# Performance work log

Measured on AMD Instinct MI355X. Metric: run time of the kernel, lower is better.

The kernel has to match this reference:

```python
import jax, jax.numpy as jnp
import numpy as np
import jax.scipy.linalg as jsl


def _rbf(X1, X2, log_lengthscale):
    # squared-exponential kernel: exp(-0.5 * ||x1 - x2||^2 / ls^2)
    ls2 = jnp.exp(2.0 * log_lengthscale)
    d2 = (jnp.sum(X1 * X1, axis=1)[:, None]
          + jnp.sum(X2 * X2, axis=1)[None, :]
          - 2.0 * (X1 @ X2.T))
    return jnp.exp(-0.5 * jnp.maximum(d2, 0.0) / ls2)


def setup_inputs() -> dict:
    key = jax.random.key(0)
    k1, k2, k3, k4, k5 = jax.random.split(key, 5)
    N, D, l, rank, N_ = 1024, 8, 4, 2, 1024
    return {
        "X": jax.random.normal(k1, (N, D), dtype=jnp.float32),
        "test_X": jax.random.normal(k2, (N_, D), dtype=jnp.float32),
        "Y": jax.random.normal(k3, (N, l), dtype=jnp.float32),
        "log_noise": jnp.zeros((l,), dtype=jnp.float32),
        "covar_factor": jax.random.normal(k4, (l, rank), dtype=jnp.float32),
        "log_var": jax.random.normal(k5, (l,), dtype=jnp.float32),
        "log_lengthscale": jnp.zeros((), dtype=jnp.float32),
    }


def reference(X, test_X, Y, log_noise, covar_factor, log_var, log_lengthscale):
    N, l = Y.shape
    N_ = test_X.shape[0]
    # IndexKernel: B B^T + diag(exp(log_var))   -> (l, l)
    task_K = covar_factor @ covar_factor.T + jnp.diag(jnp.exp(log_var))
    # per-task noise kron identity -> (N*l, N*l)
    noise = jnp.kron(jnp.diag(jnp.exp(log_noise)), jnp.eye(N, dtype=X.dtype))
    # full Kronecker covariance and its Cholesky factor
    K = jnp.kron(task_K, _rbf(X, X, log_lengthscale)) + noise
    L = jnp.linalg.cholesky(K)                       # (N*l, N*l), lower
    Kx = jnp.kron(task_K, _rbf(X, test_X, log_lengthscale))     # (N*l, N_*l)
    Kxx = jnp.kron(task_K, _rbf(test_X, test_X, log_lengthscale))  # (N_*l, N_*l)
    A = jsl.solve_triangular(L, Kx, lower=True)      # L A = Kx
    Y_vec = Y.T.reshape(-1, 1)                        # vec of Y^T, (N*l, 1)
    V = jsl.solve_triangular(L, Y_vec, lower=True)
    fmean = A.T @ V                                   # (N_*l, 1)
    fvar = Kxx - A.T @ A                              # (N_*l, N_*l)
    return fmean, fvar, noise, fmean.reshape(l, N_).T
```

## Files before the change

### kernel.cpp

```cpp
#include <hip/hip_runtime.h>
#include <math.h>

#define NN 1024
#define NM (NN*NN)
#define NB 64
#define NBLK 16
#define NW 1152
#define BIG 4096

#define OFF_FVAR  ((size_t)4096)
#define OFF_NOISE ((size_t)(4096 + 16777216))
#define OFF_M4    ((size_t)(4096 + 2*16777216))

struct GPParams {
  float tk[16];
  float E[16];
  float G[16];
  float lam[4];
};

__global__ void k_prep(const float* __restrict__ logn, const float* __restrict__ cf,
                       const float* __restrict__ logv, GPParams* __restrict__ P)
{
  if (threadIdx.x != 0 || blockIdx.x != 0) return;
  double tk[4][4], Dn[4], T[4][4], U[4][4];
  for (int a=0;a<4;a++) for (int b=0;b<4;b++){
    double s = 0.0;
    for (int r=0;r<2;r++) s += (double)cf[a*2+r]*(double)cf[b*2+r];
    if (a==b) s += exp((double)logv[a]);
    tk[a][b] = s;
  }
  for (int a=0;a<4;a++) Dn[a] = exp((double)logn[a]);
  for (int a=0;a<4;a++) for (int b=0;b<4;b++)
    T[a][b] = tk[a][b]/sqrt(Dn[a]*Dn[b]);
  for (int a=0;a<4;a++) for (int b=0;b<4;b++) U[a][b] = (a==b)?1.0:0.0;
  for (int sweep=0; sweep<40; sweep++){
    for (int p=0;p<3;p++) for (int q=p+1;q<4;q++){
      double apq = T[p][q];
      if (fabs(apq) < 1e-300) continue;
      double tau = (T[q][q]-T[p][p])/(2.0*apq);
      double t = (tau >= 0.0) ? 1.0/(tau + sqrt(1.0+tau*tau))
                              : 1.0/(tau - sqrt(1.0+tau*tau));
      double c = 1.0/sqrt(1.0+t*t), s = t*c;
      for (int k=0;k<4;k++){ double akp=T[k][p], akq=T[k][q];
        T[k][p]=c*akp - s*akq; T[k][q]=s*akp + c*akq; }
      for (int k=0;k<4;k++){ double apk=T[p][k], aqk=T[q][k];
        T[p][k]=c*apk - s*aqk; T[q][k]=s*apk + c*aqk; }
      for (int k=0;k<4;k++){ double ukp=U[k][p], ukq=U[k][q];
        U[k][p]=c*ukp - s*ukq; U[k][q]=s*ukp + c*ukq; }
    }
  }
  double E[4][4], G[4][4];
  for (int a=0;a<4;a++) for (int i=0;i<4;i++) E[a][i] = U[a][i]/sqrt(Dn[a]);
  for (int a=0;a<4;a++) for (int i=0;i<4;i++){
    double s=0; for (int b=0;b<4;b++) s += tk[a][b]*E[b][i];
    G[a][i]=s;
  }
  for (int a=0;a<4;a++) for (int b=0;b<4;b++){
    P->tk[a*4+b] = (float)tk[a][b];
    P->E [a*4+b] = (float)E[a][b];
    P->G [a*4+b] = (float)G[a][b];
  }
  for (int i=0;i<4;i++){
    double l = T[i][i];
    P->lam[i] = (float)(l > 0.0 ? l : 0.0);
  }
}

__global__ void k_rbf(const float* __restrict__ X1, const float* __restrict__ X2,
                      const float* __restrict__ logls, float* __restrict__ out)
{
  __shared__ float x1s[16][8];
  __shared__ float x2s[16][8];
  int tx = threadIdx.x, ty = threadIdx.y;
  int tid = ty*16 + tx;
  if (tid < 128){
    int r = tid>>3, d = tid&7;
    x1s[r][d] = X1[((size_t)blockIdx.y*16 + r)*8 + d];
  } else {
    int t2 = tid-128, r = t2>>3, d = t2&7;
    x2s[r][d] = X2[((size_t)blockIdx.x*16 + r)*8 + d];
  }
  __syncthreads();
  float ls2 = expf(2.0f*logls[0]);
  float d2 = 0.f;
  #pragma unroll
  for (int d=0; d<8; d++){ float df = x1s[ty][d]-x2s[tx][d]; d2 += df*df; }
  int i = blockIdx.y*16+ty, j = blockIdx.x*16+tx;
  out[(size_t)i*NN + j] = expf(-0.5f*d2/ls2);
}

__global__ void k_rbfM(const float* __restrict__ X1, const float* __restrict__ logls,
                       const GPParams* __restrict__ P, float* __restrict__ M)
{
  __shared__ float x1s[16][8];
  __shared__ float x2s[16][8];
  int tx = threadIdx.x, ty = threadIdx.y;
  int tid = ty*16 + tx;
  if (tid < 128){
    int r = tid>>3, d = tid&7;
    x1s[r][d] = X1[((size_t)blockIdx.y*16 + r)*8 + d];
  } else {
    int t2 = tid-128, r = t2>>3, d = t2&7;
    x2s[r][d] = X1[((size_t)blockIdx.x*16 + r)*8 + d];
  }
  __syncthreads();
  float ls2 = expf(2.0f*logls[0]);
  float d2 = 0.f;
  #pragma unroll
  for (int d=0; d<8; d++){ float df = x1s[ty][d]-x2s[tx][d]; d2 += df*df; }
  int i = blockIdx.y*16+ty, j = blockIdx.x*16+tx;
  float v = expf(-0.5f*d2/ls2);
  float diag = (i==j) ? 1.f : 0.f;
  size_t idx = (size_t)i*NN + j;
  #pragma unroll
  for (int z=0;z<4;z++)
    M[(size_t)z*NM + idx] = P->lam[z]*v + diag;
}

__global__ void k_uvec(const float* __restrict__ Y, const GPParams* __restrict__ P,
                       float* __restrict__ u)
{
  int n = blockIdx.x*256 + threadIdx.x;
  float y0 = Y[n*4+0], y1 = Y[n*4+1], y2 = Y[n*4+2], y3 = Y[n*4+3];
  #pragma unroll
  for (int i=0;i<4;i++)
    u[i*NN + n] = P->E[0*4+i]*y0 + P->E[1*4+i]*y1 + P->E[2*4+i]*y2 + P->E[3*4+i]*y3;
}

__device__ __forceinline__ void gemm64(const float* __restrict__ A, const float* __restrict__ B,
                                       float acc[4][4], int r0, int c0, bool sub)
{
  for (int p=0;p<64;p++){
    float ar[4], bc[4];
    #pragma unroll
    for (int ii=0;ii<4;ii++) ar[ii]=A[(r0+ii)*65+p];
    #pragma unroll
    for (int jj=0;jj<4;jj++) bc[jj]=B[p*65+c0+jj];
    if (sub){
      #pragma unroll
      for (int ii=0;ii<4;ii++)
        #pragma unroll
        for (int jj=0;jj<4;jj++) acc[ii][jj] -= ar[ii]*bc[jj];
    } else {
      #pragma unroll
      for (int ii=0;ii<4;ii++)
        #pragma unroll
        for (int jj=0;jj<4;jj++) acc[ii][jj] += ar[ii]*bc[jj];
    }
  }
}

__global__ __launch_bounds__(256) void k_potf2(float* __restrict__ M, float* __restrict__ Linv, int k)
{
  int z = blockIdx.x, tid = threadIdx.x;
  __shared__ float a[64*65];
  __shared__ float lo[64*65];
  __shared__ float ai[32*33];
  __shared__ float bb[32*33];
  __shared__ float t1[32*33];
  float* Mz = M + (size_t)z*NM;
  int base = k*NB;
  for (int idx=tid; idx<4096; idx+=256){
    int r=idx>>6, c=idx&63;
    a[r*65+c] = Mz[(size_t)(base+r)*NN + base + c];
  }
  int r = tid & 63, q = tid >> 6;
  for (int j=0;j<64;j++){
    __syncthreads();
    float d = a[j*65+j];
    float invd = 1.f/d;
    float rs = rsqrtf(d);
    if (q==0){
      if (r == j) lo[j*65+j] = sqrtf(d);
      else if (r > j) lo[r*65+j] = a[r*65+j]*rs;
      else lo[r*65+j] = 0.f;
    }
    if (r > j){
      float lrj = a[r*65+j]*invd;
      for (int c=j+1+q; c<=r; c+=4)
        a[r*65+c] -= lrj * a[c*65+j];
    }
  }
  __syncthreads();
  if (tid < 32){
    int c = tid;
    for (int rr=0;rr<c;rr++) ai[rr*33+c]=0.f;
    for (int rr=c;rr<32;rr++){
      float s = (rr==c)?1.f:0.f;
      for (int j=c;j<rr;j++) s -= lo[rr*65+j]*ai[j*33+c];
      ai[rr*33+c] = s / lo[rr*65+rr];
    }
  } else if (tid < 64){
    int c = tid-32;
    for (int rr=0;rr<c;rr++) bb[rr*33+c]=0.f;
    for (int rr=c;rr<32;rr++){
      float s=(rr==c)?1.f:0.f;
      for (int j=c;j<rr;j++) s -= lo[(32+rr)*65+(32+j)]*bb[j*33+c];
      bb[rr*33+c] = s / lo[(32+rr)*65+(32+rr)];
    }
  }
  __syncthreads();
  for (int idx=tid; idx<1024; idx+=256){
    int rr=idx>>5, c=idx&31;
    float s=0.f;
    for (int j=0;j<32;j++) s += lo[(32+rr)*65+j]*ai[j*33+c];
    t1[rr*33+c]=s;
  }
  __syncthreads();
  float* Lg = Linv + ((size_t)z*NBLK + k)*(NB*NB);
  float* Td = Mz + (size_t)base*NN + base;
  for (int idx=tid; idx<1024; idx+=256){
    int rr=idx>>5, c=idx&31;
    float s=0.f;
    for (int j=0;j<32;j++) s += bb[rr*33+j]*t1[j*33+c];
    float q21 = -s, q11 = ai[rr*33+c], q22 = bb[rr*33+c];
    Lg[(32+rr)*64 + c]      = q21;
    Lg[rr*64 + (32+c)]      = 0.f;
    Lg[rr*64 + c]           = q11;
    Lg[(32+rr)*64 + (32+c)] = q22;
    Td[(size_t)(32+rr)*NN + c]      = q21;
    Td[(size_t)rr*NN + (32+c)]      = 0.f;
    Td[(size_t)rr*NN + c]           = q11;
    Td[(size_t)(32+rr)*NN + (32+c)] = q22;
  }
}

__global__ __launch_bounds__(256) void k_csf(float* __restrict__ M, float* __restrict__ Linv,
                                             float* __restrict__ Lbuf, int k)
{
  int z = blockIdx.z;
  int tt = blockIdx.x, i2 = 0;
  while (tt >= i2+1){ tt -= (i2+1); i2++; }
  int bi = k+1+i2, bj = k+1+tt;
  bool fblk = (i2==0);
  bool diag = (bi==bj);
  __shared__ float pa[64*65];
  __shared__ float pb[64*65];
  __shared__ float li[64*65];
  float* Mz = M + (size_t)z*NM;
  const float* Lg = Linv + ((size_t)z*NBLK + k)*(NB*NB);
  int tid = threadIdx.x;
  for (int idx=tid; idx<4096; idx+=256){
    int r=idx>>6, c=idx&63;
    li[r*65+c] = Lg[idx];
    pa[r*65+c] = Mz[(size_t)(bi*64+r)*NN + k*64 + c];
    if (fblk)       pb[r*65+c] = Mz[(size_t)(bi*64+r)*NN + bi*64 + c];
    else if (!diag) pb[r*65+c] = Mz[(size_t)(bj*64+r)*NN + k*64 + c];
  }
  __syncthreads();
  int r0 = tid & 63, qq = tid >> 6;
  float sp[16], sq[16];
  for (int s=0;s<16;s++){
    int c = qq + s*4;
    float acc=0.f;
    for (int p=0;p<=c;p++) acc += pa[r0*65+p]*li[c*65+p];
    sp[s]=acc;
  }
  if (!diag){
    for (int s=0;s<16;s++){
      int c = qq + s*4;
      float acc=0.f;
      for (int p=0;p<=c;p++) acc += pb[r0*65+p]*li[c*65+p];
      sq[s]=acc;
    }
  }
  __syncthreads();
  for (int s=0;s<16;s++){
    int c = qq + s*4;
    pa[r0*65+c]=sp[s];
    if (!diag) pb[r0*65+c]=sq[s];
  }
  __syncthreads();
  float acc[4][4] = {};
  int ty = tid>>4, tx = tid&15;
  int rr0 = ty*4, cc0 = tx*4;
  const float* pbb = diag ? pa : pb;
  for (int p=0;p<64;p++){
    float ar[4], bc[4];
    #pragma unroll
    for (int ii=0;ii<4;ii++) ar[ii]=pa[(rr0+ii)*65+p];
    #pragma unroll
    for (int jj=0;jj<4;jj++) bc[jj]=pbb[(cc0+jj)*65+p];
    #pragma unroll
    for (int ii=0;ii<4;ii++)
      #pragma unroll
      for (int jj=0;jj<4;jj++) acc[ii][jj] += ar[ii]*bc[jj];
  }

  if (!fblk){
    for (int ii=0;ii<4;ii++){
      float4* ptr = (float4*)&Mz[(size_t)(bi*64+rr0+ii)*NN + bj*64+cc0];
      float4 v = *ptr;
      v.x-=acc[ii][0]; v.y-=acc[ii][1]; v.z-=acc[ii][2]; v.w-=acc[ii][3];
      *ptr = v;
    }
    if (bj == k+1){
      float* Lb = Lbuf + (size_t)z*NM;
      for (int idx=tid; idx<4096; idx+=256){
        int r=idx>>6, c=idx&63;
        Lb[(size_t)(bi*64+r)*NN + k*64 + c] = pa[r*65+c];
      }
    }
    return;
  }

  #pragma unroll
  for (int ii=0;ii<4;ii++)
    #pragma unroll
    for (int jj=0;jj<4;jj++) pb[(rr0+ii)*65+cc0+jj] -= acc[ii][jj];
  {
    float* Lb = Lbuf + (size_t)z*NM;
    for (int idx=tid; idx<4096; idx+=256){
      int r=idx>>6, c=idx&63;
      Lb[(size_t)(bi*64+r)*NN + k*64 + c] = pa[r*65+c];
    }
  }
  int r = tid & 63, q = tid >> 6;
  for (int j=0;j<64;j++){
    __syncthreads();
    float d = pb[j*65+j];
    float invd = 1.f/d;
    float rs = rsqrtf(d);
    if (q==0){
      if (r == j) li[j*65+j] = sqrtf(d);
      else if (r > j) li[r*65+j] = pb[r*65+j]*rs;
      else li[r*65+j] = 0.f;
    }
    if (r > j){
      float lrj = pb[r*65+j]*invd;
      for (int c=j+1+q; c<=r; c+=4)
        pb[r*65+c] -= lrj * pb[c*65+j];
    }
  }
  __syncthreads();
  float* ai = pa;
  float* bb = pa + 1056;
  float* t1 = pa + 2112;
  if (tid < 32){
    int c = tid;
    for (int rr=0;rr<c;rr++) ai[rr*33+c]=0.f;
    for (int rr=c;rr<32;rr++){
      float s = (rr==c)?1.f:0.f;
      for (int j=c;j<rr;j++) s -= li[rr*65+j]*ai[j*33+c];
      ai[rr*33+c] = s / li[rr*65+rr];
    }
  } else if (tid < 64){
    int c = tid-32;
    for (int rr=0;rr<c;rr++) bb[rr*33+c]=0.f;
    for (int rr=c;rr<32;rr++){
      float s=(rr==c)?1.f:0.f;
      for (int j=c;j<rr;j++) s -= li[(32+rr)*65+(32+j)]*bb[j*33+c];
      bb[rr*33+c] = s / li[(32+rr)*65+(32+rr)];
    }
  }
  __syncthreads();
  for (int idx=tid; idx<1024; idx+=256){
    int rr=idx>>5, c=idx&31;
    float s=0.f;
    for (int j=0;j<32;j++) s += li[(32+rr)*65+j]*ai[j*33+c];
    t1[rr*33+c]=s;
  }
  __syncthreads();
  float* Lg2 = Linv + ((size_t)z*NBLK + (k+1))*(NB*NB);
  float* Td  = Mz + (size_t)(bi*64)*NN + bi*64;
  for (int idx=tid; idx<1024; idx+=256){
    int rr=idx>>5, c=idx&31;
    float s=0.f;
    for (int j=0;j<32;j++) s += bb[rr*33+j]*t1[j*33+c];
    float q21 = -s, q11 = ai[rr*33+c], q22 = bb[rr*33+c];
    Lg2[(32+rr)*64 + c]      = q21;
    Lg2[rr*64 + (32+c)]      = 0.f;
    Lg2[rr*64 + c]           = q11;
    Lg2[(32+rr)*64 + (32+c)] = q22;
    Td[(size_t)(32+rr)*NN + c]      = q21;
    Td[(size_t)rr*NN + (32+c)]      = 0.f;
    Td[(size_t)rr*NN + c]           = q11;
    Td[(size_t)(32+rr)*NN + (32+c)] = q22;
  }
}

__global__ __launch_bounds__(256) void k_dbl1(const float* __restrict__ Lbuf,
                                              const float* __restrict__ Linv,
                                              float* __restrict__ Tinv)
{
  int pair = blockIdx.x, z = blockIdx.y, tid = threadIdx.x;
  int b0 = 2*pair, b1 = 2*pair+1;
  __shared__ float l21[64*65];
  __shared__ float ai[64*65];
  __shared__ float tt[64*65];
  const float* Lb = Lbuf + (size_t)z*NM;
  const float* La = Linv + ((size_t)z*NBLK + b0)*(NB*NB);
  const float* Lc = Linv + ((size_t)z*NBLK + b1)*(NB*NB);
  for (int idx=tid; idx<4096; idx+=256){
    int r=idx>>6, c=idx&63;
    l21[r*65+c] = Lb[(size_t)(b1*64+r)*NN + b0*64 + c];
    ai[r*65+c]  = La[idx];
  }
  __syncthreads();
  int ty=tid>>4, tx=tid&15, r0=ty*4, c0=tx*4;
  float acc[4][4]={};
  gemm64(l21, ai, acc, r0, c0, false);
  __syncthreads();
  #pragma unroll
  for (int ii=0;ii<4;ii++)
    #pragma unroll
    for (int jj=0;jj<4;jj++) tt[(r0+ii)*65 + c0+jj] = acc[ii][jj];
  for (int idx=tid; idx<4096; idx+=256){
    int r=idx>>6, c=idx&63;
    ai[r*65+c] = Lc[idx];
  }
  __syncthreads();
  float fin[4][4]={};
  gemm64(ai, tt, fin, r0, c0, false);
  float* Tz = Tinv + (size_t)z*NM;
  #pragma unroll
  for (int ii=0;ii<4;ii++){
    float4 v = make_float4(-fin[ii][0],-fin[ii][1],-fin[ii][2],-fin[ii][3]);
    *(float4*)&Tz[(size_t)(b1*64+r0+ii)*NN + b0*64+c0] = v;
  }
}

__global__ __launch_bounds__(256) void k_dblT(const float* __restrict__ Lbuf,
                                              const float* __restrict__ Tinv,
                                              float* __restrict__ tb, int g64)
{
  int z = blockIdx.y, tid = threadIdx.x;
  int tpp = g64*g64;
  int pair = blockIdx.x / tpp;
  int tt2 = blockIdx.x % tpp;
  int ti = tt2 / g64, tj = tt2 % g64;
  int b0 = 2*pair*g64, b1 = b0 + g64;
  const float* Lb = Lbuf + (size_t)z*NM;
  const float* Tz = Tinv + (size_t)z*NM;
  __shared__ float lt[64*65];
  __shared__ float rt[64*65];
  int ty=tid>>4, tx=tid&15, r0=ty*4, c0=tx*4;
  float acc[4][4]={};
  for (int kb=tj; kb<g64; kb++){
    for (int idx=tid; idx<4096; idx+=256){
      int r=idx>>6, c=idx&63;
      lt[r*65+c] = Lb[(size_t)((b1+ti)*64+r)*NN + (b0+kb)*64 + c];
      rt[r*65+c] = Tz[(size_t)((b0+kb)*64+r)*NN + (b0+tj)*64 + c];
    }
    __syncthreads();
    gemm64(lt, rt, acc, r0, c0, false);
    __syncthreads();
  }
  int g = g64*64;
  float* tz = tb + (size_t)z*262144 + (size_t)pair*g*g;
  #pragma unroll
  for (int ii=0;ii<4;ii++){
    float4 v = make_float4(acc[ii][0],acc[ii][1],acc[ii][2],acc[ii][3]);
    *(float4*)&tz[(size_t)(ti*64+r0+ii)*g + tj*64+c0] = v;
  }
}

__global__ __launch_bounds__(256) void k_dblC(const float* __restrict__ tb,
                                              float* __restrict__ Tinv, int g64)
{
  int z = blockIdx.y, tid = threadIdx.x;
  int tpp = g64*g64;
  int pair = blockIdx.x / tpp;
  int tt2 = blockIdx.x % tpp;
  int ti = tt2 / g64, tj = tt2 % g64;
  int b0 = 2*pair*g64, b1 = b0 + g64;
  float* Tz = Tinv + (size_t)z*NM;
  int g = g64*64;
  const float* tz = tb + (size_t)z*262144 + (size_t)pair*g*g;
  __shared__ float lt[64*65];
  __shared__ float rt[64*65];
  int ty=tid>>4, tx=tid&15, r0=ty*4, c0=tx*4;
  float acc[4][4]={};
  for (int kb=0; kb<=ti; kb++){
    for (int idx=tid; idx<4096; idx+=256){
      int r=idx>>6, c=idx&63;
      lt[r*65+c] = Tz[(size_t)((b1+ti)*64+r)*NN + (b1+kb)*64 + c];
      rt[r*65+c] = tz[(size_t)(kb*64+r)*g + tj*64 + c];
    }
    __syncthreads();
    gemm64(lt, rt, acc, r0, c0, false);
    __syncthreads();
  }
  #pragma unroll
  for (int ii=0;ii<4;ii++){
    float4 v = make_float4(-acc[ii][0],-acc[ii][1],-acc[ii][2],-acc[ii][3]);
    *(float4*)&Tz[(size_t)((b1+ti)*64+r0+ii)*NN + b0*64+tj*64+c0] = v;
  }
}

__global__ __launch_bounds__(256) void k_wgemm(const float* __restrict__ Tinv,
                                               const float* __restrict__ R,
                                               const float* __restrict__ u,
                                               float* __restrict__ W)
{
  int ct = blockIdx.x;
  int bi = blockIdx.y;
  int z  = blockIdx.z;
  const float* Tz = Tinv + (size_t)z*NM;
  float* Wz = W + (size_t)z*NN*NW;
  __shared__ float At[64*68];
  __shared__ float Bs[64*132];
  int tid = threadIdx.x;
  int ty = tid>>4, tx = tid&15;
  float areg[16], breg[32];
  float acc[4][8] = {};
  #pragma unroll
  for (int i=0;i<16;i++){
    int idx=i*256+tid, r=idx>>6, c=idx&63;
    areg[i] = Tz[(size_t)(bi*64+r)*NN + c];
  }
  #pragma unroll
  for (int i=0;i<32;i++){
    int idx=i*256+tid, r=idx>>7, c=idx&127;
    breg[i] = (ct<8) ? R[(size_t)r*NN + ct*128 + c]
                     : ((c<4) ? u[c*NN + r] : 0.f);
  }
  for (int kb=0; kb<=bi; kb++){
    __syncthreads();
    #pragma unroll
    for (int i=0;i<16;i++){
      int idx=i*256+tid, r=idx>>6, c=idx&63;
      At[c*68 + r] = areg[i];
    }
    #pragma unroll
    for (int i=0;i<32;i++){
      int idx=i*256+tid, r=idx>>7, c=idx&127;
      Bs[r*132 + c] = breg[i];
    }
    if (kb < bi){
      int kn = kb+1;
      #pragma unroll
      for (int i=0;i<16;i++){
        int idx=i*256+tid, r=idx>>6, c=idx&63;
        areg[i] = Tz[(size_t)(bi*64+r)*NN + kn*64 + c];
      }
      #pragma unroll
      for (int i=0;i<32;i++){
        int idx=i*256+tid, r=idx>>7, c=idx&127;
        int gr = kn*64 + r;
        breg[i] = (ct<8) ? R[(size_t)gr*NN + ct*128 + c]
                         : ((c<4) ? u[c*NN + gr] : 0.f);
      }
    }
    __syncthreads();
    for (int p=0;p<64;p++){
      float4 a4 = *(const float4*)&At[p*68 + ty*4];
      float4 b0 = *(const float4*)&Bs[p*132 + tx*8];
      float4 b1 = *(const float4*)&Bs[p*132 + tx*8 + 4];
      float ar[4]={a4.x,a4.y,a4.z,a4.w};
      float bc[8]={b0.x,b0.y,b0.z,b0.w,b1.x,b1.y,b1.z,b1.w};
      #pragma unroll
      for (int ii=0;ii<4;ii++)
        #pragma unroll
        for (int jj=0;jj<8;jj++) acc[ii][jj] += ar[ii]*bc[jj];
    }
  }
  #pragma unroll
  for (int ii=0;ii<4;ii++){
    size_t row = (size_t)(bi*64 + ty*4 + ii)*NW + ct*128 + tx*8;
    *(float4*)&Wz[row]   = make_float4(acc[ii][0],acc[ii][1],acc[ii][2],acc[ii][3]);
    *(float4*)&Wz[row+4] = make_float4(acc[ii][4],acc[ii][5],acc[ii][6],acc[ii][7]);
  }
}

__global__ __launch_bounds__(256) void k_WtW(const float* __restrict__ W,
                                             float* __restrict__ Qa, float* __restrict__ Qb)
{
  int z = blockIdx.z;
  int ks = blockIdx.x / 36;
  int tt = blockIdx.x % 36, mi = 0;
  while (tt >= mi+1){ tt -= (mi+1); mi++; }
  int mj = tt;
  const float* Wz = W + (size_t)z*NN*NW;
  float* Qz = (ks ? Qb : Qa) + (size_t)z*NM;
  int mi0 = mi*128, mj0 = mj*128;
  __shared__ float as[16*132];
  __shared__ float bs[16*132];
  int tid = threadIdx.x;
  int ty = tid>>4, tx = tid&15;
  float areg[8], breg[8];
  float acc[8][8] = {};
  int nbase = ks*512;
  #pragma unroll
  for (int i=0;i<8;i++){
    int idx=i*256+tid, r=idx>>7, c=idx&127;
    areg[i] = Wz[(size_t)(nbase+r)*NW + mi0 + c];
    breg[i] = Wz[(size_t)(nbase+r)*NW + mj0 + c];
  }
  for (int s=0;s<32;s++){
    __syncthreads();
    #pragma unroll
    for (int i=0;i<8;i++){
      int idx=i*256+tid, r=idx>>7, c=idx&127;
      as[r*132+c]=areg[i];
      bs[r*132+c]=breg[i];
    }
    if (s<31){
      int n0 = nbase + (s+1)*16;
      #pragma unroll
      for (int i=0;i<8;i++){
        int idx=i*256+tid, r=idx>>7, c=idx&127;
        areg[i] = Wz[(size_t)(n0+r)*NW + mi0 + c];
        breg[i] = Wz[(size_t)(n0+r)*NW + mj0 + c];
      }
    }
    __syncthreads();
    #pragma unroll
    for (int p=0;p<16;p++){
      float4 a0 = *(const float4*)&as[p*132 + ty*8];
      float4 a1 = *(const float4*)&as[p*132 + ty*8 + 4];
      float4 b0 = *(const float4*)&bs[p*132 + tx*8];
      float4 b1 = *(const float4*)&bs[p*132 + tx*8 + 4];
      float arf[8]={a0.x,a0.y,a0.z,a0.w,a1.x,a1.y,a1.z,a1.w};
      float bcf[8]={b0.x,b0.y,b0.z,b0.w,b1.x,b1.y,b1.z,b1.w};
      #pragma unroll
      for (int ii=0;ii<8;ii++)
        #pragma unroll
        for (int jj=0;jj<8;jj++) acc[ii][jj]+=arf[ii]*bcf[jj];
    }
  }
  for (int ii=0;ii<8;ii++){
    size_t row = (size_t)(mi0 + ty*8 + ii)*NN + mj0 + tx*8;
    *(float4*)&Qz[row]   = make_float4(acc[ii][0],acc[ii][1],acc[ii][2],acc[ii][3]);
    *(float4*)&Qz[row+4] = make_float4(acc[ii][4],acc[ii][5],acc[ii][6],acc[ii][7]);
  }
  if (mi != mj){
    for (int jj=0;jj<8;jj++){
      size_t row = (size_t)(mj0 + tx*8 + jj)*NN + mi0 + ty*8;
      *(float4*)&Qz[row]   = make_float4(acc[0][jj],acc[1][jj],acc[2][jj],acc[3][jj]);
      *(float4*)&Qz[row+4] = make_float4(acc[4][jj],acc[5][jj],acc[6][jj],acc[7][jj]);
    }
  }
}

__global__ void k_colmul(const float* __restrict__ W, float* __restrict__ wpart)
{
  int mc = blockIdx.x, z = blockIdx.y, ns = blockIdx.z, tid = threadIdx.x;
  __shared__ float ufs[256];
  const float* Wz = W + (size_t)z*NN*NW;
  ufs[tid] = Wz[(size_t)(ns*256+tid)*NW + 1024 + z];
  __syncthreads();
  int m = mc*256 + tid;
  float acc = 0.f;
  for (int n=0;n<256;n++)
    acc += Wz[(size_t)(ns*256+n)*NW + m]*ufs[n];
  wpart[(size_t)(z*4+ns)*1024 + m] = acc;
}

__global__ void k_fmeanout(const float* __restrict__ wpart, const GPParams* __restrict__ P,
                           float* __restrict__ out)
{
  int m = blockIdx.x*256 + threadIdx.x;
  float w[4];
  #pragma unroll
  for (int i=0;i<4;i++){
    float s=0.f;
    #pragma unroll
    for (int ns=0;ns<4;ns++) s += wpart[(size_t)(i*4+ns)*1024 + m];
    w[i]=s;
  }
  #pragma unroll
  for (int a=0;a<4;a++){
    float fm = 0.f;
    #pragma unroll
    for (int i=0;i<4;i++) fm += P->G[a*4+i]*w[i];
    out[a*NN + m] = fm;
    out[OFF_M4 + (size_t)m*4 + a] = fm;
  }
}

__global__ void k_fvar(const float* __restrict__ S, const float* __restrict__ Qa,
                       const float* __restrict__ Qb, const GPParams* __restrict__ P,
                       float* __restrict__ out)
{
  size_t idx = (size_t)blockIdx.x*256 + threadIdx.x;
  int m = (int)(idx>>10), mp = (int)(idx & 1023);
  float s = S[idx];
  float q[4];
  #pragma unroll
  for (int i=0;i<4;i++) q[i] = Qa[(size_t)i*NM + idx] + Qb[(size_t)i*NM + idx];
  float* fv = out + OFF_FVAR;
  #pragma unroll
  for (int a=0;a<4;a++)
    #pragma unroll
    for (int b=0;b<4;b++){
      float val = P->tk[a*4+b]*s;
      #pragma unroll
      for (int i=0;i<4;i++) val -= P->G[a*4+i]*P->G[b*4+i]*q[i];
      fv[(size_t)(a*NN+m)*BIG + (size_t)b*NN + mp] = val;
    }
}

__global__ void k_noise(const float* __restrict__ logn, float* __restrict__ out)
{
  size_t idx = (size_t)blockIdx.x*256 + threadIdx.x;
  int row = (int)(idx>>12), col = (int)(idx & 4095);
  out[OFF_NOISE + idx] = (row==col) ? expf(logn[row>>10]) : 0.f;
}

extern "C" void kernel_launch(void* const* d_in, const int* in_sizes, int n_in,
                              void* d_out, int out_size, void* d_ws, size_t ws_size,
                              hipStream_t stream)
{
  const float* X    = (const float*)d_in[0];
  const float* tX   = (const float*)d_in[1];
  const float* Y    = (const float*)d_in[2];
  const float* logn = (const float*)d_in[3];
  const float* cf   = (const float*)d_in[4];
  const float* logv = (const float*)d_in[5];
  const float* logls= (const float*)d_in[6];
  float* out = (float*)d_out;

  size_t need_floats = 64 + 4096 + 16384
                     + 2*(size_t)NM + 4*(size_t)NM + 262144 + 4*(size_t)NM
                     + 4*(size_t)NN*NW;
  float* base;
  if (ws_size >= (need_floats + 1024)*sizeof(float)) base = (float*)d_ws;
  else base = out + OFF_NOISE;

  GPParams* P  = (GPParams*)base;
  float* u     = base + 64;
  float* wpart = u + 4096;
  float* R     = wpart + 16384;
  float* S     = R + NM;
  float* M     = S + NM;
  float* Linv  = M + 4*(size_t)NM;
  float* Lbuf  = Linv + 262144;
  float* W     = Lbuf + 4*(size_t)NM;
  float* Tinv  = M;
  float* Qa    = M;
  float* Qb    = Lbuf;
  float* tb    = W;

  dim3 b16(16,16);

  k_prep<<<1, 1, 0, stream>>>(logn, cf, logv, P);
  k_rbf <<<dim3(64,64), b16, 0, stream>>>(X,  tX, logls, R);
  k_rbf <<<dim3(64,64), b16, 0, stream>>>(tX, tX, logls, S);
  k_rbfM<<<dim3(64,64), b16, 0, stream>>>(X, logls, P, M);
  k_uvec<<<dim3(4), 256, 0, stream>>>(Y, P, u);

  k_potf2<<<dim3(4), 256, 0, stream>>>(M, Linv, 0);
  for (int k=0;k<NBLK-1;k++){
    int nb = NBLK-1-k;
    k_csf<<<dim3(nb*(nb+1)/2, 1, 4), 256, 0, stream>>>(M, Linv, Lbuf, k);
  }

  k_dbl1<<<dim3(8,4), 256, 0, stream>>>(Lbuf, Linv, Tinv);
  for (int g64=2; g64<=8; g64*=2){
    int np = 8/g64;
    k_dblT<<<dim3(np*g64*g64, 4), 256, 0, stream>>>(Lbuf, Tinv, tb, g64);
    k_dblC<<<dim3(np*g64*g64, 4), 256, 0, stream>>>(tb, Tinv, g64);
  }

  k_wgemm<<<dim3(9,16,4), 256, 0, stream>>>(Tinv, R, u, W);

  k_WtW<<<dim3(72,1,4), 256, 0, stream>>>(W, Qa, Qb);
  k_colmul<<<dim3(4,4,4), 256, 0, stream>>>(W, wpart);
  k_fmeanout<<<dim3(4), 256, 0, stream>>>(wpart, P, out);
  k_fvar<<<dim3(NM/256), 256, 0, stream>>>(S, Qa, Qb, P, out);
  k_noise<<<dim3(16777216/256), 256, 0, stream>>>(logn, out);
}
```

Measured before the change: 2.296 ms.

## Use precomputed Linv^T Linv for trailing updates and split-K WtW with atomics

The right-looking blocked Cholesky now precomputes G = Linv_k^T Linv_k for each diagonal block. Trailing-update blocks then compute A_i G A_j^T with dense 64x64 GEMMs instead of triangular solves on both panels. Panel solves are done only where L is actually stored: the first sub-diagonal block and the bj==k+1 column. Separately, the WtW reduction is split four ways along K and accumulated with atomicAdd into a zeroed Q, which doubles parallelism but adds a zeroing pass, atomic traffic, nondeterministic summation order, and extra flops in the Cholesky.

```diff
diff --git a/kernel.cpp b/kernel.cpp
--- a/kernel.cpp
+++ b/kernel.cpp
@@ -150,8 +150,24 @@
     }
   }
 }
-
-__global__ __launch_bounds__(256) void k_potf2(float* __restrict__ M, float* __restrict__ Linv, int k)
+__device__ __forceinline__ void gemm64T(const float* __restrict__ A, const float* __restrict__ B,
+                                        float acc[4][4], int r0, int c0)
+{
+  for (int p=0;p<64;p++){
+    float ar[4], bc[4];
+    #pragma unroll
+    for (int ii=0;ii<4;ii++) ar[ii]=A[(r0+ii)*65+p];
+    #pragma unroll
+    for (int jj=0;jj<4;jj++) bc[jj]=B[(c0+jj)*65+p];
+    #pragma unroll
+    for (int ii=0;ii<4;ii++)
+      #pragma unroll
+      for (int jj=0;jj<4;jj++) acc[ii][jj] += ar[ii]*bc[jj];
+  }
+}
+
+__global__ __launch_bounds__(256) void k_potf2(float* __restrict__ M, float* __restrict__ Linv,
+                                               float* __restrict__ Gbuf, int k)
 {
   int z = blockIdx.x, tid = threadIdx.x;
   __shared__ float a[64*65];
@@ -223,160 +239,204 @@
     Td[(size_t)rr*NN + (32+c)]      = 0.f;
     Td[(size_t)rr*NN + c]           = q11;
     Td[(size_t)(32+rr)*NN + (32+c)] = q22;
+    a[(32+rr)*65 + c]      = q21;
+    a[rr*65 + (32+c)]      = 0.f;
+    a[rr*65 + c]           = q11;
+    a[(32+rr)*65 + (32+c)] = q22;
+  }
+  __syncthreads();
+  {
+    int r0=(tid>>4)*4, c0=(tid&15)*4;
+    float g[4][4]={};
+    for (int p=0;p<64;p++){
+      float ar[4], bc[4];
+      #pragma unroll
+      for (int ii=0;ii<4;ii++) ar[ii]=a[p*65+r0+ii];
+      #pragma unroll
+      for (int jj=0;jj<4;jj++) bc[jj]=a[p*65+c0+jj];
+      #pragma unroll
+      for (int ii=0;ii<4;ii++)
+        #pragma unroll
+        for (int jj=0;jj<4;jj++) g[ii][jj]+=ar[ii]*bc[jj];
+    }
+    float* Gg = Gbuf + ((size_t)z*NBLK + k)*4096;
+    #pragma unroll
+    for (int ii=0;ii<4;ii++)
+      *(float4*)&Gg[(r0+ii)*64 + c0] = make_float4(g[ii][0],g[ii][1],g[ii][2],g[ii][3]);
   }
 }
 
 __global__ __launch_bounds__(256) void k_csf(float* __restrict__ M, float* __restrict__ Linv,
-                                             float* __restrict__ Lbuf, int k)
+                                             float* __restrict__ Gbuf, float* __restrict__ Lbuf, int k)
 {
   int z = blockIdx.z;
   int tt = blockIdx.x, i2 = 0;
   while (tt >= i2+1){ tt -= (i2+1); i2++; }
   int bi = k+1+i2, bj = k+1+tt;
   bool fblk = (i2==0);
-  bool diag = (bi==bj);
   __shared__ float pa[64*65];
   __shared__ float pb[64*65];
   __shared__ float li[64*65];
   float* Mz = M + (size_t)z*NM;
-  const float* Lg = Linv + ((size_t)z*NBLK + k)*(NB*NB);
+  float* Lb = Lbuf + (size_t)z*NM;
   int tid = threadIdx.x;
+  int ty = tid>>4, tx = tid&15;
+  int r0 = ty*4, c0 = tx*4;
+
+  if (fblk){
+    const float* Lg = Linv + ((size_t)z*NBLK + k)*(NB*NB);
+    for (int idx=tid; idx<4096; idx+=256){
+      int r=idx>>6, c=idx&63;
+      li[r*65+c] = Lg[idx];
+      pa[r*65+c] = Mz[(size_t)(bi*64+r)*NN + k*64 + c];
+      pb[r*65+c] = Mz[(size_t)(bi*64+r)*NN + bi*64 + c];
+    }
+    __syncthreads();
+    float sc[4][4]={};
+    gemm64T(pa, li, sc, r0, c0);
+    #pragma unroll
+    for (int ii=0;ii<4;ii++)
+      *(float4*)&Lb[(size_t)(bi*64+r0+ii)*NN + k*64+c0] =
+        make_float4(sc[ii][0],sc[ii][1],sc[ii][2],sc[ii][3]);
+    __syncthreads();
+    #pragma unroll
+    for (int ii=0;ii<4;ii++)
+      #pragma unroll
+      for (int jj=0;jj<4;jj++) pa[(r0+ii)*65+c0+jj] = sc[ii][jj];
+    __syncthreads();
+    float upd[4][4]={};
+    gemm64T(pa, pa, upd, r0, c0);
+    #pragma unroll
+    for (int ii=0;ii<4;ii++)
+      #pragma unroll
+      for (int jj=0;jj<4;jj++) pb[(r0+ii)*65+c0+jj] -= upd[ii][jj];
+    int r = tid & 63, q = tid >> 6;
+    for (int j=0;j<64;j++){
+      __syncthreads();
+      float d = pb[j*65+j];
+      float invd = 1.f/d;
+      float rs = rsqrtf(d);
+      if (q==0){
+        if (r == j) li[j*65+j] = sqrtf(d);
+        else if (r > j) li[r*65+j] = pb[r*65+j]*rs;
+        else li[r*65+j] = 0.f;
+      }
+      if (r > j){
+        float lrj = pb[r*65+j]*invd;
+        for (int c=j+1+q; c<=r; c+=4)
+          pb[r*65+c] -= lrj * pb[c*65+j];
+      }
+    }
+    __syncthreads();
+    float* ai = pa;
+    float* bbv = pa + 1056;
+    float* t1 = pa + 2112;
+    if (tid < 32){
+      int c = tid;
+      for (int rr=0;rr<c;rr++) ai[rr*33+c]=0.f;
+      for (int rr=c;rr<32;rr++){
+        float s = (rr==c)?1.f:0.f;
+        for (int j=c;j<rr;j++) s -= li[rr*65+j]*ai[j*33+c];
+        ai[rr*33+c] = s / li[rr*65+rr];
+      }
+    } else if (tid < 64){
+      int c = tid-32;
+      for (int rr=0;rr<c;rr++) bbv[rr*33+c]=0.f;
+      for (int rr=c;rr<32;rr++){
+        float s=(rr==c)?1.f:0.f;
+        for (int j=c;j<rr;j++) s -= li[(32+rr)*65+(32+j)]*bbv[j*33+c];
+        bbv[rr*33+c] = s / li[(32+rr)*65+(32+rr)];
+      }
+    }
+    __syncthreads();
+    for (int idx=tid; idx<1024; idx+=256){
+      int rr=idx>>5, c=idx&31;
+      float s=0.f;
+      for (int j=0;j<32;j++) s += li[(32+rr)*65+j]*ai[j*33+c];
+      t1[rr*33+c]=s;
+    }
+    __syncthreads();
+    float* Lg2 = Linv + ((size_t)z*NBLK + (k+1))*(NB*NB);
+    float* Td  = Mz + (size_t)(bi*64)*NN + bi*64;
+    for (int idx=tid; idx<1024; idx+=256){
+      int rr=idx>>5, c=idx&31;
+      float s=0.f;
+      for (int j=0;j<32;j++) s += bbv[rr*33+j]*t1[j*33+c];
+      float q21 = -s, q11 = ai[rr*33+c], q22 = bbv[rr*33+c];
+      Lg2[(32+rr)*64 + c]      = q21;
+      Lg2[rr*64 + (32+c)]      = 0.f;
+      Lg2[rr*64 + c]           = q11;
+      Lg2[(32+rr)*64 + (32+c)] = q22;
+      Td[(size_t)(32+rr)*NN + c]      = q21;
+      Td[(size_t)rr*NN + (32+c)]      = 0.f;
+      Td[(size_t)rr*NN + c]           = q11;
+      Td[(size_t)(32+rr)*NN + (32+c)] = q22;
+      pb[(32+rr)*65 + c]      = q21;
+      pb[rr*65 + (32+c)]      = 0.f;
+      pb[rr*65 + c]           = q11;
+      pb[(32+rr)*65 + (32+c)] = q22;
+    }
+    __syncthreads();
+    {
+      float g[4][4]={};
+      for (int p=0;p<64;p++){
+        float ar[4], bc[4];
+        #pragma unroll
+        for (int ii=0;ii<4;ii++) ar[ii]=pb[p*65+r0+ii];
+        #pragma unroll
+        for (int jj=0;jj<4;jj++) bc[jj]=pb[p*65+c0+jj];
+        #pragma unroll
+        for (int ii=0;ii<4;ii++)
+          #pragma unroll
+          for (int jj=0;jj<4;jj++) g[ii][jj]+=ar[ii]*bc[jj];
+      }
+      float* Gg = Gbuf + ((size_t)z*NBLK + (k+1))*4096;
+      #pragma unroll
+      for (int ii=0;ii<4;ii++)
+        *(float4*)&Gg[(r0+ii)*64 + c0] = make_float4(g[ii][0],g[ii][1],g[ii][2],g[ii][3]);
+    }
+    return;
+  }
+
+  const float* Gg = Gbuf + ((size_t)z*NBLK + k)*4096;
   for (int idx=tid; idx<4096; idx+=256){
     int r=idx>>6, c=idx&63;
-    li[r*65+c] = Lg[idx];
+    li[r*65+c] = Gg[idx];
     pa[r*65+c] = Mz[(size_t)(bi*64+r)*NN + k*64 + c];
-    if (fblk)       pb[r*65+c] = Mz[(size_t)(bi*64+r)*NN + bi*64 + c];
-    else if (!diag) pb[r*65+c] = Mz[(size_t)(bj*64+r)*NN + k*64 + c];
-  }
-  __syncthreads();
-  int r0 = tid & 63, qq = tid >> 6;
-  float sp[16], sq[16];
-  for (int s=0;s<16;s++){
-    int c = qq + s*4;
-    float acc=0.f;
-    for (int p=0;p<=c;p++) acc += pa[r0*65+p]*li[c*65+p];
-    sp[s]=acc;
-  }
-  if (!diag){
-    for (int s=0;s<16;s++){
-      int c = qq + s*4;
-      float acc=0.f;
-      for (int p=0;p<=c;p++) acc += pb[r0*65+p]*li[c*65+p];
-      sq[s]=acc;
-    }
-  }
-  __syncthreads();
-  for (int s=0;s<16;s++){
-    int c = qq + s*4;
-    pa[r0*65+c]=sp[s];
-    if (!diag) pb[r0*65+c]=sq[s];
-  }
-  __syncthreads();
-  float acc[4][4] = {};
-  int ty = tid>>4, tx = tid&15;
-  int rr0 = ty*4, cc0 = tx*4;
-  const float* pbb = diag ? pa : pb;
-  for (int p=0;p<64;p++){
-    float ar[4], bc[4];
-    #pragma unroll
-    for (int ii=0;ii<4;ii++) ar[ii]=pa[(rr0+ii)*65+p];
-    #pragma unroll
-    for (int jj=0;jj<4;jj++) bc[jj]=pbb[(cc0+jj)*65+p];
-    #pragma unroll
-    for (int ii=0;ii<4;ii++)
-      #pragma unroll
-      for (int jj=0;jj<4;jj++) acc[ii][jj] += ar[ii]*bc[jj];
-  }
-
-  if (!fblk){
-    for (int ii=0;ii<4;ii++){
-      float4* ptr = (float4*)&Mz[(size_t)(bi*64+rr0+ii)*NN + bj*64+cc0];
-      float4 v = *ptr;
-      v.x-=acc[ii][0]; v.y-=acc[ii][1]; v.z-=acc[ii][2]; v.w-=acc[ii][3];
-      *ptr = v;
-    }
-    if (bj == k+1){
-      float* Lb = Lbuf + (size_t)z*NM;
-      for (int idx=tid; idx<4096; idx+=256){
-        int r=idx>>6, c=idx&63;
-        Lb[(size_t)(bi*64+r)*NN + k*64 + c] = pa[r*65+c];
-      }
-    }
-    return;
-  }
-
+    pb[r*65+c] = Mz[(size_t)(bj*64+r)*NN + k*64 + c];
+  }
+  __syncthreads();
+  float t[4][4]={};
+  gemm64(pa, li, t, r0, c0, false);
+  __syncthreads();
   #pragma unroll
   for (int ii=0;ii<4;ii++)
     #pragma unroll
-    for (int jj=0;jj<4;jj++) pb[(rr0+ii)*65+cc0+jj] -= acc[ii][jj];
-  {
-    float* Lb = Lbuf + (size_t)z*NM;
+    for (int jj=0;jj<4;jj++) li[(r0+ii)*65+c0+jj] = t[ii][jj];
+  __syncthreads();
+  float upd[4][4]={};
+  gemm64T(li, pb, upd, r0, c0);
+  #pragma unroll
+  for (int ii=0;ii<4;ii++){
+    float4* ptr = (float4*)&Mz[(size_t)(bi*64+r0+ii)*NN + bj*64+c0];
+    float4 v = *ptr;
+    v.x-=upd[ii][0]; v.y-=upd[ii][1]; v.z-=upd[ii][2]; v.w-=upd[ii][3];
+    *ptr = v;
+  }
+  if (bj == k+1){
+    __syncthreads();
+    const float* Lg = Linv + ((size_t)z*NBLK + k)*(NB*NB);
     for (int idx=tid; idx<4096; idx+=256){
       int r=idx>>6, c=idx&63;
-      Lb[(size_t)(bi*64+r)*NN + k*64 + c] = pa[r*65+c];
-    }
-  }
-  int r = tid & 63, q = tid >> 6;
-  for (int j=0;j<64;j++){
-    __syncthreads();
-    float d = pb[j*65+j];
-    float invd = 1.f/d;
-    float rs = rsqrtf(d);
-    if (q==0){
-      if (r == j) li[j*65+j] = sqrtf(d);
-      else if (r > j) li[r*65+j] = pb[r*65+j]*rs;
-      else li[r*65+j] = 0.f;
-    }
-    if (r > j){
-      float lrj = pb[r*65+j]*invd;
-      for (int c=j+1+q; c<=r; c+=4)
-        pb[r*65+c] -= lrj * pb[c*65+j];
-    }
-  }
-  __syncthreads();
-  float* ai = pa;
-  float* bb = pa + 1056;
-  float* t1 = pa + 2112;
-  if (tid < 32){
-    int c = tid;
-    for (int rr=0;rr<c;rr++) ai[rr*33+c]=0.f;
-    for (int rr=c;rr<32;rr++){
-      float s = (rr==c)?1.f:0.f;
-      for (int j=c;j<rr;j++) s -= li[rr*65+j]*ai[j*33+c];
-      ai[rr*33+c] = s / li[rr*65+rr];
-    }
-  } else if (tid < 64){
-    int c = tid-32;
-    for (int rr=0;rr<c;rr++) bb[rr*33+c]=0.f;
-    for (int rr=c;rr<32;rr++){
-      float s=(rr==c)?1.f:0.f;
-      for (int j=c;j<rr;j++) s -= li[(32+rr)*65+(32+j)]*bb[j*33+c];
-      bb[rr*33+c] = s / li[(32+rr)*65+(32+rr)];
-    }
-  }
-  __syncthreads();
-  for (int idx=tid; idx<1024; idx+=256){
-    int rr=idx>>5, c=idx&31;
-    float s=0.f;
-    for (int j=0;j<32;j++) s += li[(32+rr)*65+j]*ai[j*33+c];
-    t1[rr*33+c]=s;
-  }
-  __syncthreads();
-  float* Lg2 = Linv + ((size_t)z*NBLK + (k+1))*(NB*NB);
-  float* Td  = Mz + (size_t)(bi*64)*NN + bi*64;
-  for (int idx=tid; idx<1024; idx+=256){
-    int rr=idx>>5, c=idx&31;
-    float s=0.f;
-    for (int j=0;j<32;j++) s += bb[rr*33+j]*t1[j*33+c];
-    float q21 = -s, q11 = ai[rr*33+c], q22 = bb[rr*33+c];
-    Lg2[(32+rr)*64 + c]      = q21;
-    Lg2[rr*64 + (32+c)]      = 0.f;
-    Lg2[rr*64 + c]           = q11;
-    Lg2[(32+rr)*64 + (32+c)] = q22;
-    Td[(size_t)(32+rr)*NN + c]      = q21;
-    Td[(size_t)rr*NN + (32+c)]      = 0.f;
-    Td[(size_t)rr*NN + c]           = q11;
-    Td[(size_t)(32+rr)*NN + (32+c)] = q22;
+      pb[r*65+c] = Lg[idx];
+    }
+    __syncthreads();
+    float sc[4][4]={};
+    gemm64T(pa, pb, sc, r0, c0);
+    #pragma unroll
+    for (int ii=0;ii<4;ii++)
+      *(float4*)&Lb[(size_t)(bi*64+r0+ii)*NN + k*64+c0] =
+        make_float4(sc[ii][0],sc[ii][1],sc[ii][2],sc[ii][3]);
   }
 }
 
@@ -564,8 +624,13 @@
   }
 }
 
-__global__ __launch_bounds__(256) void k_WtW(const float* __restrict__ W,
-                                             float* __restrict__ Qa, float* __restrict__ Qb)
+__global__ void k_zeroQ(float* __restrict__ Q)
+{
+  size_t i = ((size_t)blockIdx.x*256 + threadIdx.x)*4;
+  *(float4*)&Q[i] = make_float4(0.f,0.f,0.f,0.f);
+}
+
+__global__ __launch_bounds__(256) void k_WtW(const float* __restrict__ W, float* __restrict__ Q)
 {
   int z = blockIdx.z;
   int ks = blockIdx.x / 36;
@@ -573,7 +638,7 @@
   while (tt >= mi+1){ tt -= (mi+1); mi++; }
   int mj = tt;
   const float* Wz = W + (size_t)z*NN*NW;
-  float* Qz = (ks ? Qb : Qa) + (size_t)z*NM;
+  float* Qz = Q + (size_t)z*NM;
   int mi0 = mi*128, mj0 = mj*128;
   __shared__ float as[16*132];
   __shared__ float bs[16*132];
@@ -581,14 +646,14 @@
   int ty = tid>>4, tx = tid&15;
   float areg[8], breg[8];
   float acc[8][8] = {};
-  int nbase = ks*512;
+  int nbase = ks*256;
   #pragma unroll
   for (int i=0;i<8;i++){
     int idx=i*256+tid, r=idx>>7, c=idx&127;
     areg[i] = Wz[(size_t)(nbase+r)*NW + mi0 + c];
     breg[i] = Wz[(size_t)(nbase+r)*NW + mj0 + c];
   }
-  for (int s=0;s<32;s++){
+  for (int s=0;s<16;s++){
     __syncthreads();
     #pragma unroll
     for (int i=0;i<8;i++){
@@ -596,7 +661,7 @@
       as[r*132+c]=areg[i];
       bs[r*132+c]=breg[i];
     }
-    if (s<31){
+    if (s<15){
       int n0 = nbase + (s+1)*16;
       #pragma unroll
       for (int i=0;i<8;i++){
@@ -622,14 +687,14 @@
   }
   for (int ii=0;ii<8;ii++){
     size_t row = (size_t)(mi0 + ty*8 + ii)*NN + mj0 + tx*8;
-    *(float4*)&Qz[row]   = make_float4(acc[ii][0],acc[ii][1],acc[ii][2],acc[ii][3]);
-    *(float4*)&Qz[row+4] = make_float4(acc[ii][4],acc[ii][5],acc[ii][6],acc[ii][7]);
+    #pragma unroll
+    for (int jj=0;jj<8;jj++) atomicAdd(&Qz[row+jj], acc[ii][jj]);
   }
   if (mi != mj){
     for (int jj=0;jj<8;jj++){
       size_t row = (size_t)(mj0 + tx*8 + jj)*NN + mi0 + ty*8;
-      *(float4*)&Qz[row]   = make_float4(acc[0][jj],acc[1][jj],acc[2][jj],acc[3][jj]);
-      *(float4*)&Qz[row+4] = make_float4(acc[4][jj],acc[5][jj],acc[6][jj],acc[7][jj]);
+      #pragma unroll
+      for (int ii=0;ii<8;ii++) atomicAdd(&Qz[row+ii], acc[ii][jj]);
     }
   }
 }
@@ -670,16 +735,15 @@
   }
 }
 
-__global__ void k_fvar(const float* __restrict__ S, const float* __restrict__ Qa,
-                       const float* __restrict__ Qb, const GPParams* __restrict__ P,
-                       float* __restrict__ out)
+__global__ void k_fvar(const float* __restrict__ S, const float* __restrict__ Q,
+                       const GPParams* __restrict__ P, float* __restrict__ out)
 {
   size_t idx = (size_t)blockIdx.x*256 + threadIdx.x;
   int m = (int)(idx>>10), mp = (int)(idx & 1023);
   float s = S[idx];
   float q[4];
   #pragma unroll
-  for (int i=0;i<4;i++) q[i] = Qa[(size_t)i*NM + idx] + Qb[(size_t)i*NM + idx];
+  for (int i=0;i<4;i++) q[i] = Q[(size_t)i*NM + idx];
   float* fv = out + OFF_FVAR;
   #pragma unroll
   for (int a=0;a<4;a++)
@@ -713,7 +777,7 @@
   float* out = (float*)d_out;
 
   size_t need_floats = 64 + 4096 + 16384
-                     + 2*(size_t)NM + 4*(size_t)NM + 262144 + 4*(size_t)NM
+                     + 2*(size_t)NM + 4*(size_t)NM + 262144 + 262144 + 4*(size_t)NM
                      + 4*(size_t)NN*NW;
   float* base;
   if (ws_size >= (need_floats + 1024)*sizeof(float)) base = (float*)d_ws;
@@ -726,11 +790,11 @@
   float* S     = R + NM;
   float* M     = S + NM;
   float* Linv  = M + 4*(size_t)NM;
-  float* Lbuf  = Linv + 262144;
+  float* Gbuf  = Linv + 262144;
+  float* Lbuf  = Gbuf + 262144;
   float* W     = Lbuf + 4*(size_t)NM;
   float* Tinv  = M;
-  float* Qa    = M;
-  float* Qb    = Lbuf;
+  float* Q     = Lbuf;
   float* tb    = W;
 
   dim3 b16(16,16);
@@ -741,10 +805,10 @@
   k_rbfM<<<dim3(64,64), b16, 0, stream>>>(X, logls, P, M);
   k_uvec<<<dim3(4), 256, 0, stream>>>(Y, P, u);
 
-  k_potf2<<<dim3(4), 256, 0, stream>>>(M, Linv, 0);
+  k_potf2<<<dim3(4), 256, 0, stream>>>(M, Linv, Gbuf, 0);
   for (int k=0;k<NBLK-1;k++){
     int nb = NBLK-1-k;
-    k_csf<<<dim3(nb*(nb+1)/2, 1, 4), 256, 0, stream>>>(M, Linv, Lbuf, k);
+    k_csf<<<dim3(nb*(nb+1)/2, 1, 4), 256, 0, stream>>>(M, Linv, Gbuf, Lbuf, k);
   }
 
   k_dbl1<<<dim3(8,4), 256, 0, stream>>>(Lbuf, Linv, Tinv);
@@ -756,9 +820,11 @@
 
   k_wgemm<<<dim3(9,16,4), 256, 0, stream>>>(Tinv, R, u, W);
 
-  k_WtW<<<dim3(72,1,4), 256, 0, stream>>>(W, Qa, Qb);
+  k_zeroQ<<<dim3(4096), 256, 0, stream>>>(Q);
+  k_WtW<<<dim3(144,1,4), 256, 0, stream>>>(W, Q);
+
   k_colmul<<<dim3(4,4,4), 256, 0, stream>>>(W, wpart);
   k_fmeanout<<<dim3(4), 256, 0, stream>>>(wpart, P, out);
-  k_fvar<<<dim3(NM/256), 256, 0, stream>>>(S, Qa, Qb, P, out);
+  k_fvar<<<dim3(NM/256), 256, 0, stream>>>(S, Q, P, out);
   k_noise<<<dim3(16777216/256), 256, 0, stream>>>(logn, out);
 }
```

New measurement: 2.541 ms. +10.7%, slower.
